# Optimization experiments

Hardware: AMD Instinct MI355X
Metric: run time of the kernel (lower is better)

Reference implementation:

```python
import jax, jax.numpy as jnp
import numpy as np

KERNEL_MUL = 2.0
KERNEL_NUM = 5


def _mmd(source, target):
    n_s = source.shape[0]
    total = jnp.concatenate([source, target], axis=0)  # (2N, D)
    n = total.shape[0]
    # pairwise squared L2 via a^2 + b^2 - 2ab (avoids (2N,2N,D) intermediate)
    sq = jnp.sum(total * total, axis=1)  # (2N,)
    L2 = sq[:, None] + sq[None, :] - 2.0 * (total @ total.T)  # (2N, 2N)
    # torch uses L2_distance.data for bandwidth -> stop_gradient
    bandwidth = jax.lax.stop_gradient(jnp.sum(L2)) / (n * n - n)
    bandwidth = bandwidth / (KERNEL_MUL ** (KERNEL_NUM // 2))
    # multi-bandwidth RBF sum
    kernels = jnp.zeros_like(L2)
    for i in range(KERNEL_NUM):
        kernels = kernels + jnp.exp(-L2 / (bandwidth * KERNEL_MUL ** i))
    XX = kernels[:n_s, :n_s]
    YY = kernels[n_s:, n_s:]
    XY = kernels[:n_s, n_s:]
    YX = kernels[n_s:, :n_s]
    return jnp.mean(XX) + jnp.mean(YY) - jnp.mean(XY) - jnp.mean(YX)


def setup_inputs() -> dict:
    key = jax.random.key(0)
    k1, k2 = jax.random.split(key)
    source = jax.random.normal(k1, (4096, 256), dtype=jnp.float32)
    target = jax.random.normal(k2, (4096, 256), dtype=jnp.float32) + 0.5
    return {"source": source, "target": target}


def reference(source, target):
    return _mmd(source, target)
```

## Files before the change

kernel.cpp:

```cpp
#include <hip/hip_runtime.h>

typedef short bf16x8 __attribute__((ext_vector_type(8)));
typedef float f32x4 __attribute__((ext_vector_type(4)));

#define KDIM 256
#define BT 128
#define BK 64

__device__ __forceinline__ unsigned short f2bf(float f) {
  unsigned u = __float_as_uint(f);
  unsigned r = (u + 0x7fffu + ((u >> 16) & 1u)) >> 16;
  return (unsigned short)r;
}
__device__ __forceinline__ float bf2f(unsigned short b) {
  return __uint_as_float(((unsigned)b) << 16);
}

__device__ __forceinline__ void async_cp16(const void* g, void* l) {
  __builtin_amdgcn_global_load_lds(
      (const __attribute__((address_space(1))) unsigned int*)g,
      (__attribute__((address_space(3))) unsigned int*)l, 16, 0, 0);
}

__global__ __launch_bounds__(256) void mmd_stage(
    const float* __restrict__ src, const float* __restrict__ tgt, int ns,
    unsigned short* __restrict__ Tbf, float* __restrict__ sq,
    float* __restrict__ scol, float* __restrict__ sum_sq) {
  __shared__ float sp[256];
  __shared__ float rw[4];
  int t = threadIdx.x;
  int lane = t & 63, wave = t >> 6;
  sp[t] = 0.f;
  __syncthreads();
  int sub = t & 31;
  int rsel = t >> 5;
  float colacc[8];
#pragma unroll
  for (int j = 0; j < 8; ++j) colacc[j] = 0.f;
  float tsq = 0.f;
#pragma unroll
  for (int it = 0; it < 4; ++it) {
    int r = blockIdx.x * 32 + it * 8 + rsel;
    const float* rp = (r < ns) ? (src + (size_t)r * KDIM)
                               : (tgt + (size_t)(r - ns) * KDIM);
    float4 v0 = *(const float4*)(rp + sub * 8);
    float4 v1 = *(const float4*)(rp + sub * 8 + 4);
    float vals[8] = {v0.x, v0.y, v0.z, v0.w, v1.x, v1.y, v1.z, v1.w};
    unsigned pk[4];
    float ssp = 0.f;
#pragma unroll
    for (int j = 0; j < 4; ++j) {
      unsigned short b0 = f2bf(vals[2 * j]);
      unsigned short b1 = f2bf(vals[2 * j + 1]);
      float x0 = bf2f(b0), x1 = bf2f(b1);
      pk[j] = (unsigned)b0 | ((unsigned)b1 << 16);
      ssp += x0 * x0 + x1 * x1;
      colacc[2 * j] += x0;
      colacc[2 * j + 1] += x1;
    }
    *(uint4*)(Tbf + (size_t)r * KDIM + sub * 8) =
        make_uint4(pk[0], pk[1], pk[2], pk[3]);
    tsq += ssp;
    float ss = ssp;
#pragma unroll
    for (int off = 16; off; off >>= 1) ss += __shfl_down(ss, off, 32);
    if (sub == 0) sq[r] = ss;
  }
#pragma unroll
  for (int j = 0; j < 8; ++j) atomicAdd(&sp[sub * 8 + j], colacc[j]);
#pragma unroll
  for (int off = 32; off; off >>= 1) tsq += __shfl_down(tsq, off, 64);
  if (lane == 0) rw[wave] = tsq;
  __syncthreads();
  atomicAdd(&scol[t], sp[t]);
  if (t == 0) atomicAdd(sum_sq, rw[0] + rw[1] + rw[2] + rw[3]);
}

__global__ void mmd_prep2(const float* __restrict__ scol,
                          const float* __restrict__ sum_sq,
                          float* __restrict__ coef, float* __restrict__ out,
                          int n) {
  int t = threadIdx.x;
  float4 v = *(const float4*)(scol + t * 4);
  float p = v.x * v.x + v.y * v.y + v.z * v.z + v.w * v.w;
#pragma unroll
  for (int off = 32; off; off >>= 1) p += __shfl_down(p, off, 64);
  if (t == 0) {
    double ssq = (double)p;
    double S = (double)sum_sq[0];
    double nn = (double)n;
    double sumL2 = 2.0 * nn * S - 2.0 * ssq;
    double bw = sumL2 / (nn * nn - nn) / 4.0;
    double l2e = 1.4426950408889634;
#pragma unroll
    for (int i = 0; i < 5; ++i)
      coef[i] = (float)(-l2e / (bw * (double)(1 << i)));
    out[0] = 0.f;
  }
}

__device__ __forceinline__ float2 pk_add(float2 a, float2 b) {
  return make_float2(a.x + b.x, a.y + b.y);
}
__device__ __forceinline__ float2 pk_mul(float2 a, float2 b) {
  return make_float2(a.x * b.x, a.y * b.y);
}
__device__ __forceinline__ float2 pk_fma(float2 a, float2 b, float2 c) {
  return make_float2(__builtin_fmaf(a.x, b.x, c.x),
                     __builtin_fmaf(a.y, b.y, c.y));
}

__global__ __launch_bounds__(256) void mmd_main(
    const unsigned short* __restrict__ Tbf, const float* __restrict__ sq,
    const float* __restrict__ coef, float* __restrict__ out, int halfTiles,
    float inv) {
  __shared__ short As[BT * BK];
  __shared__ short Bs[BT * BK];
  __shared__ float sqa[BT];
  __shared__ float sqb[BT];
  __shared__ float red[4];

  int id = blockIdx.x;
  int bi = (int)((sqrtf(8.f * (float)id + 1.f) - 1.f) * 0.5f);
  while ((bi + 1) * (bi + 2) / 2 <= id) ++bi;
  while (bi * (bi + 1) / 2 > id) --bi;
  int bj = id - bi * (bi + 1) / 2;
  int rowBase = bi * BT, colBase = bj * BT;

  int t = threadIdx.x;
  int lane = t & 63, wave = t >> 6;

  if (t < 128) sqa[t] = sq[rowBase + t];
  else sqb[t - 128] = sq[colBase + (t - 128)];

  f32x4 acc[4][4];
#pragma unroll
  for (int a = 0; a < 4; ++a)
#pragma unroll
    for (int b = 0; b < 4; ++b) {
      f32x4 z = {0.f, 0.f, 0.f, 0.f};
      acc[a][b] = z;
    }

  int wrow = (wave >> 1) * 64, wcol = (wave & 1) * 64;
  int lrow = lane >> 3;
  int kgsw = (lane & 7) ^ lrow;
  int frow = lane & 15;
  int kq = lane >> 4;

  for (int c = 0; c < 4; ++c) {
    int k0 = c * BK;
#pragma unroll
    for (int j = 0; j < 4; ++j) {
      int R0 = j * 32 + wave * 8;
      int ldsoff = (j * 256 + wave * 64) * 8;
      async_cp16(Tbf + (size_t)(rowBase + R0 + lrow) * KDIM + k0 + kgsw * 8,
                 &As[ldsoff]);
      async_cp16(Tbf + (size_t)(colBase + R0 + lrow) * KDIM + k0 + kgsw * 8,
                 &Bs[ldsoff]);
    }
    __syncthreads();
#pragma unroll
    for (int ks = 0; ks < 2; ++ks) {
      bf16x8 af[4], bfv[4];
#pragma unroll
      for (int mt = 0; mt < 4; ++mt) {
        int r = wrow + mt * 16 + frow;
        int pg = (ks * 4 + kq) ^ (r & 7);
        af[mt] = *(const bf16x8*)&As[r * BK + pg * 8];
      }
#pragma unroll
      for (int nt = 0; nt < 4; ++nt) {
        int r = wcol + nt * 16 + frow;
        int pg = (ks * 4 + kq) ^ (r & 7);
        bfv[nt] = *(const bf16x8*)&Bs[r * BK + pg * 8];
      }
#pragma unroll
      for (int mt = 0; mt < 4; ++mt)
#pragma unroll
        for (int nt = 0; nt < 4; ++nt)
          acc[mt][nt] = __builtin_amdgcn_mfma_f32_16x16x32_bf16(
              af[mt], bfv[nt], acc[mt][nt], 0, 0, 0);
    }
    __syncthreads();
  }

  float c4 = coef[4];
  float m2c4 = -2.f * c4;
  float2 m2v = make_float2(m2c4, m2c4);
  int ccol = lane & 15;
  int rb = (lane >> 4) * 4;
  float ra[16];
#pragma unroll
  for (int mt = 0; mt < 4; ++mt)
#pragma unroll
    for (int rg = 0; rg < 4; ++rg)
      ra[mt * 4 + rg] = sqa[wrow + mt * 16 + rb + rg] * c4;
  float cbv[4];
#pragma unroll
  for (int nt = 0; nt < 4; ++nt) cbv[nt] = sqb[wcol + nt * 16 + ccol] * c4;

  float2 lsum2 = make_float2(0.f, 0.f);
#pragma unroll
  for (int mt = 0; mt < 4; ++mt) {
#pragma unroll
    for (int nt = 0; nt < 4; ++nt) {
      float cb = cbv[nt];
#pragma unroll
      for (int rp = 0; rp < 4; rp += 2) {
        float2 g = make_float2(acc[mt][nt][rp], acc[mt][nt][rp + 1]);
        float2 sab = make_float2(ra[mt * 4 + rp] + cb, ra[mt * 4 + rp + 1] + cb);
        float2 u = pk_fma(g, m2v, sab);
        float2 e = make_float2(__builtin_amdgcn_exp2f(u.x),
                               __builtin_amdgcn_exp2f(u.y));
        float2 e2 = pk_mul(e, e);
        float2 e4 = pk_mul(e2, e2);
        float2 e8 = pk_mul(e4, e4);
        float2 s = pk_add(e, e2);
        s = pk_add(s, e4);
        s = pk_add(s, e8);
        s = pk_fma(e8, e8, s);
        lsum2 = pk_add(lsum2, s);
      }
    }
  }
  float lsum = lsum2.x + lsum2.y;
#pragma unroll
  for (int off = 32; off; off >>= 1) lsum += __shfl_down(lsum, off, 64);
  if (lane == 0) red[wave] = lsum;
  __syncthreads();
  if (t == 0) {
    float w = ((bi < halfTiles) == (bj < halfTiles)) ? 1.f : -1.f;
    float f = (bi == bj) ? 1.f : 2.f;
    atomicAdd(out, w * f * inv * (red[0] + red[1] + red[2] + red[3]));
  }
}

extern "C" void kernel_launch(void* const* d_in, const int* in_sizes, int n_in,
                              void* d_out, int out_size, void* d_ws,
                              size_t ws_size, hipStream_t stream) {
  const float* src = (const float*)d_in[0];
  const float* tgt = (const float*)d_in[1];
  int ns = in_sizes[0] / KDIM;
  int ntr = in_sizes[1] / KDIM;
  int n = ns + ntr;

  char* ws = (char*)d_ws;
  unsigned short* Tbf = (unsigned short*)ws;
  size_t off = (size_t)n * KDIM * sizeof(unsigned short);
  float* sq = (float*)(ws + off);     off += (size_t)n * 4;
  float* scol = (float*)(ws + off);   off += (size_t)KDIM * 4;
  float* sum_sq = (float*)(ws + off); off += 4;
  float* coef = (float*)(ws + off);

  hipMemsetAsync(scol, 0, (KDIM + 1) * sizeof(float), stream);

  mmd_stage<<<n / 32, 256, 0, stream>>>(src, tgt, ns, Tbf, sq, scol, sum_sq);
  mmd_prep2<<<1, 64, 0, stream>>>(scol, sum_sq, coef, (float*)d_out, n);
  int nb = n / BT;
  int nblk = nb * (nb + 1) / 2;
  mmd_main<<<nblk, 256, 0, stream>>>(Tbf, sq, coef, (float*)d_out, ns / BT,
                                     1.f / ((float)ns * (float)ns));
}
```

Measured before the change: 110.9 us.

## Fuse stage, bandwidth reduction and main tile loop into one cooperative persistent kernel

```diff
diff --git a/kernel.cpp b/kernel.cpp
--- a/kernel.cpp
+++ b/kernel.cpp
@@ -1,4 +1,7 @@
 #include <hip/hip_runtime.h>
+#include <hip/hip_cooperative_groups.h>
+
+namespace cg = cooperative_groups;
 
 typedef short bf16x8 __attribute__((ext_vector_type(8)));
 typedef float f32x4 __attribute__((ext_vector_type(4)));
@@ -20,6 +23,242 @@
   __builtin_amdgcn_global_load_lds(
       (const __attribute__((address_space(1))) unsigned int*)g,
       (__attribute__((address_space(3))) unsigned int*)l, 16, 0, 0);
+}
+
+__device__ __forceinline__ float2 pk_add(float2 a, float2 b) {
+  return make_float2(a.x + b.x, a.y + b.y);
+}
+__device__ __forceinline__ float2 pk_mul(float2 a, float2 b) {
+  return make_float2(a.x * b.x, a.y * b.y);
+}
+__device__ __forceinline__ float2 pk_fma(float2 a, float2 b, float2 c) {
+  return make_float2(__builtin_fmaf(a.x, b.x, c.x),
+                     __builtin_fmaf(a.y, b.y, c.y));
+}
+
+__global__ __launch_bounds__(256) void mmd_fused(
+    const float* __restrict__ src, const float* __restrict__ tgt, int ns,
+    unsigned short* __restrict__ Tbf, float* __restrict__ sq,
+    float* __restrict__ pscol, float* __restrict__ psums,
+    float* __restrict__ p2col, float* __restrict__ p2s,
+    float* __restrict__ out, int halfTiles, float inv, int nTiles,
+    int nChunks, int n) {
+  __shared__ short As[BT * BK];
+  __shared__ short Bs[BT * BK];
+  __shared__ float sqa[BT];
+  __shared__ float sqb[BT];
+  __shared__ float redS[4];
+  __shared__ float coefS;
+
+  cg::grid_group grid = cg::this_grid();
+  int t = threadIdx.x;
+  int lane = t & 63, wave = t >> 6;
+  int nB = gridDim.x;
+  int blk = blockIdx.x;
+
+  float* sp = (float*)As;
+  sp[t] = 0.f;
+  __syncthreads();
+  int sub = t & 31;
+  int rsel = t >> 5;
+  float colacc[8];
+#pragma unroll
+  for (int j = 0; j < 8; ++j) colacc[j] = 0.f;
+  float tsq = 0.f;
+  for (int cs = blk; cs < nChunks; cs += nB) {
+    int r = cs * 8 + rsel;
+    const float* rp = (r < ns) ? (src + (size_t)r * KDIM)
+                               : (tgt + (size_t)(r - ns) * KDIM);
+    float4 v0 = *(const float4*)(rp + sub * 8);
+    float4 v1 = *(const float4*)(rp + sub * 8 + 4);
+    float vals[8] = {v0.x, v0.y, v0.z, v0.w, v1.x, v1.y, v1.z, v1.w};
+    unsigned pk[4];
+    float ssp = 0.f;
+#pragma unroll
+    for (int j = 0; j < 4; ++j) {
+      unsigned short b0 = f2bf(vals[2 * j]);
+      unsigned short b1 = f2bf(vals[2 * j + 1]);
+      float x0 = bf2f(b0), x1 = bf2f(b1);
+      pk[j] = (unsigned)b0 | ((unsigned)b1 << 16);
+      ssp += x0 * x0 + x1 * x1;
+      colacc[2 * j] += x0;
+      colacc[2 * j + 1] += x1;
+    }
+    *(uint4*)(Tbf + (size_t)r * KDIM + sub * 8) =
+        make_uint4(pk[0], pk[1], pk[2], pk[3]);
+    tsq += ssp;
+    float ss = ssp;
+#pragma unroll
+    for (int off = 16; off; off >>= 1) ss += __shfl_down(ss, off, 32);
+    if (sub == 0) sq[r] = ss;
+  }
+#pragma unroll
+  for (int j = 0; j < 8; ++j) atomicAdd(&sp[sub * 8 + j], colacc[j]);
+#pragma unroll
+  for (int off = 32; off; off >>= 1) tsq += __shfl_down(tsq, off, 64);
+  if (lane == 0) redS[wave] = tsq;
+  __syncthreads();
+  pscol[(size_t)blk * 256 + t] = sp[t];
+  if (t == 0) psums[blk] = redS[0] + redS[1] + redS[2] + redS[3];
+  if (blk == 0 && t == 0) out[0] = 0.f;
+  grid.sync();
+
+  int nred = (nB < 64) ? nB : 64;
+  if (blk < nred) {
+    float a = 0.f;
+    for (int r = blk; r < nB; r += 64) a += pscol[(size_t)r * 256 + t];
+    p2col[blk * 256 + t] = a;
+    if (wave == 0) {
+      float v = 0.f;
+      int r = blk + lane * 64;
+      if (lane < 16 && r < nB) v = psums[r];
+#pragma unroll
+      for (int off = 8; off; off >>= 1) v += __shfl_down(v, off, 64);
+      if (lane == 0) p2s[blk] = v;
+    }
+  }
+  grid.sync();
+
+  {
+    float s = 0.f;
+#pragma unroll 8
+    for (int r = 0; r < nred; ++r) s += p2col[r * 256 + t];
+    float p = s * s;
+#pragma unroll
+    for (int off = 32; off; off >>= 1) p += __shfl_down(p, off, 64);
+    if (lane == 0) redS[wave] = p;
+    float S = 0.f;
+    if (wave == 0) {
+      float v = (lane < nred) ? p2s[lane] : 0.f;
+#pragma unroll
+      for (int off = 32; off; off >>= 1) v += __shfl_down(v, off, 64);
+      S = v;
+    }
+    __syncthreads();
+    if (t == 0) {
+      double ssq = (double)(redS[0] + redS[1] + redS[2] + redS[3]);
+      double Sd = (double)S;
+      double nn = (double)n;
+      double sumL2 = 2.0 * nn * Sd - 2.0 * ssq;
+      double bw = sumL2 / (nn * nn - nn) / 4.0;
+      coefS = (float)(-1.4426950408889634 / (16.0 * bw));
+    }
+    __syncthreads();
+  }
+
+  int wrow = (wave >> 1) * 64, wcol = (wave & 1) * 64;
+  int lrow = lane >> 3;
+  int kgsw = (lane & 7) ^ lrow;
+  int frow = lane & 15;
+  int kq = lane >> 4;
+  int ccol = lane & 15;
+  int rb = (lane >> 4) * 4;
+
+  for (int id = blk; id < nTiles; id += nB) {
+    int bi = (int)((sqrtf(8.f * (float)id + 1.f) - 1.f) * 0.5f);
+    while ((bi + 1) * (bi + 2) / 2 <= id) ++bi;
+    while (bi * (bi + 1) / 2 > id) --bi;
+    int bj = id - bi * (bi + 1) / 2;
+    int rowBase = bi * BT, colBase = bj * BT;
+
+    if (t < 128) sqa[t] = sq[rowBase + t];
+    else sqb[t - 128] = sq[colBase + (t - 128)];
+
+    f32x4 acc[4][4];
+#pragma unroll
+    for (int a = 0; a < 4; ++a)
+#pragma unroll
+      for (int b = 0; b < 4; ++b) {
+        f32x4 z = {0.f, 0.f, 0.f, 0.f};
+        acc[a][b] = z;
+      }
+
+    for (int c = 0; c < 4; ++c) {
+      int k0 = c * BK;
+#pragma unroll
+      for (int j = 0; j < 4; ++j) {
+        int R0 = j * 32 + wave * 8;
+        int ldsoff = (j * 256 + wave * 64) * 8;
+        async_cp16(Tbf + (size_t)(rowBase + R0 + lrow) * KDIM + k0 + kgsw * 8,
+                   &As[ldsoff]);
+        async_cp16(Tbf + (size_t)(colBase + R0 + lrow) * KDIM + k0 + kgsw * 8,
+                   &Bs[ldsoff]);
+      }
+      __syncthreads();
+#pragma unroll
+      for (int ks = 0; ks < 2; ++ks) {
+        bf16x8 af[4], bfv[4];
+#pragma unroll
+        for (int mt = 0; mt < 4; ++mt) {
+          int r = wrow + mt * 16 + frow;
+          int pg = (ks * 4 + kq) ^ (r & 7);
+          af[mt] = *(const bf16x8*)&As[r * BK + pg * 8];
+        }
+#pragma unroll
+        for (int nt = 0; nt < 4; ++nt) {
+          int r = wcol + nt * 16 + frow;
+          int pg = (ks * 4 + kq) ^ (r & 7);
+          bfv[nt] = *(const bf16x8*)&Bs[r * BK + pg * 8];
+        }
+#pragma unroll
+        for (int mt = 0; mt < 4; ++mt)
+#pragma unroll
+          for (int nt = 0; nt < 4; ++nt)
+            acc[mt][nt] = __builtin_amdgcn_mfma_f32_16x16x32_bf16(
+                af[mt], bfv[nt], acc[mt][nt], 0, 0, 0);
+      }
+      __syncthreads();
+    }
+
+    float c4 = coefS;
+    float m2c4 = -2.f * c4;
+    float2 m2v = make_float2(m2c4, m2c4);
+    float ra[16];
+#pragma unroll
+    for (int mt = 0; mt < 4; ++mt)
+#pragma unroll
+      for (int rg = 0; rg < 4; ++rg)
+        ra[mt * 4 + rg] = sqa[wrow + mt * 16 + rb + rg] * c4;
+    float cbv[4];
+#pragma unroll
+    for (int nt = 0; nt < 4; ++nt) cbv[nt] = sqb[wcol + nt * 16 + ccol] * c4;
+
+    float2 lsum2 = make_float2(0.f, 0.f);
+#pragma unroll
+    for (int mt = 0; mt < 4; ++mt) {
+#pragma unroll
+      for (int nt = 0; nt < 4; ++nt) {
+        float cb = cbv[nt];
+#pragma unroll
+        for (int rp = 0; rp < 4; rp += 2) {
+          float2 g = make_float2(acc[mt][nt][rp], acc[mt][nt][rp + 1]);
+          float2 sab =
+              make_float2(ra[mt * 4 + rp] + cb, ra[mt * 4 + rp + 1] + cb);
+          float2 u = pk_fma(g, m2v, sab);
+          float2 e = make_float2(__builtin_amdgcn_exp2f(u.x),
+                                 __builtin_amdgcn_exp2f(u.y));
+          float2 e2 = pk_mul(e, e);
+          float2 e4 = pk_mul(e2, e2);
+          float2 e8 = pk_mul(e4, e4);
+          float2 s = pk_add(e, e2);
+          s = pk_add(s, e4);
+          s = pk_add(s, e8);
+          s = pk_fma(e8, e8, s);
+          lsum2 = pk_add(lsum2, s);
+        }
+      }
+    }
+    float lsum = lsum2.x + lsum2.y;
+#pragma unroll
+    for (int off = 32; off; off >>= 1) lsum += __shfl_down(lsum, off, 64);
+    if (lane == 0) redS[wave] = lsum;
+    __syncthreads();
+    if (t == 0) {
+      float w = ((bi < halfTiles) == (bj < halfTiles)) ? 1.f : -1.f;
+      float f = (bi == bj) ? 1.f : 2.f;
+      atomicAdd(out, w * f * inv * (redS[0] + redS[1] + redS[2] + redS[3]));
+    }
+  }
 }
 
 __global__ __launch_bounds__(256) void mmd_stage(
@@ -32,8 +271,7 @@
   int lane = t & 63, wave = t >> 6;
   sp[t] = 0.f;
   __syncthreads();
-  int sub = t & 31;
-  int rsel = t >> 5;
+  int sub = t & 31, rsel = t >> 5;
   float colacc[8];
 #pragma unroll
   for (int j = 0; j < 8; ++j) colacc[j] = 0.f;
@@ -91,23 +329,9 @@
     double nn = (double)n;
     double sumL2 = 2.0 * nn * S - 2.0 * ssq;
     double bw = sumL2 / (nn * nn - nn) / 4.0;
-    double l2e = 1.4426950408889634;
-#pragma unroll
-    for (int i = 0; i < 5; ++i)
-      coef[i] = (float)(-l2e / (bw * (double)(1 << i)));
+    coef[0] = (float)(-1.4426950408889634 / (16.0 * bw));
     out[0] = 0.f;
   }
-}
-
-__device__ __forceinline__ float2 pk_add(float2 a, float2 b) {
-  return make_float2(a.x + b.x, a.y + b.y);
-}
-__device__ __forceinline__ float2 pk_mul(float2 a, float2 b) {
-  return make_float2(a.x * b.x, a.y * b.y);
-}
-__device__ __forceinline__ float2 pk_fma(float2 a, float2 b, float2 c) {
-  return make_float2(__builtin_fmaf(a.x, b.x, c.x),
-                     __builtin_fmaf(a.y, b.y, c.y));
 }
 
 __global__ __launch_bounds__(256) void mmd_main(
@@ -185,7 +409,7 @@
     __syncthreads();
   }
 
-  float c4 = coef[4];
+  float c4 = coef[0];
   float m2c4 = -2.f * c4;
   float2 m2v = make_float2(m2c4, m2c4);
   int ccol = lane & 15;
@@ -209,7 +433,8 @@
 #pragma unroll
       for (int rp = 0; rp < 4; rp += 2) {
         float2 g = make_float2(acc[mt][nt][rp], acc[mt][nt][rp + 1]);
-        float2 sab = make_float2(ra[mt * 4 + rp] + cb, ra[mt * 4 + rp + 1] + cb);
+        float2 sab =
+            make_float2(ra[mt * 4 + rp] + cb, ra[mt * 4 + rp + 1] + cb);
         float2 u = pk_fma(g, m2v, sab);
         float2 e = make_float2(__builtin_amdgcn_exp2f(u.x),
                                __builtin_amdgcn_exp2f(u.y));
@@ -248,17 +473,40 @@
   char* ws = (char*)d_ws;
   unsigned short* Tbf = (unsigned short*)ws;
   size_t off = (size_t)n * KDIM * sizeof(unsigned short);
-  float* sq = (float*)(ws + off);     off += (size_t)n * 4;
-  float* scol = (float*)(ws + off);   off += (size_t)KDIM * 4;
-  float* sum_sq = (float*)(ws + off); off += 4;
-  float* coef = (float*)(ws + off);
-
-  hipMemsetAsync(scol, 0, (KDIM + 1) * sizeof(float), stream);
-
-  mmd_stage<<<n / 32, 256, 0, stream>>>(src, tgt, ns, Tbf, sq, scol, sum_sq);
-  mmd_prep2<<<1, 64, 0, stream>>>(scol, sum_sq, coef, (float*)d_out, n);
+  float* sq = (float*)(ws + off);    off += (size_t)n * 4;
+  float* pscol = (float*)(ws + off); off += (size_t)1024 * 256 * 4;
+  float* psums = (float*)(ws + off); off += 1024 * 4;
+  float* p2col = (float*)(ws + off); off += 64 * 256 * 4;
+  float* p2s = (float*)(ws + off);   off += 64 * 4;
+  float* scolF = (float*)(ws + off); off += 256 * 4;
+  float* sumsqF = (float*)(ws + off); off += 4;
+  float* coefF = (float*)(ws + off);
+
+  float* out = (float*)d_out;
   int nb = n / BT;
-  int nblk = nb * (nb + 1) / 2;
-  mmd_main<<<nblk, 256, 0, stream>>>(Tbf, sq, coef, (float*)d_out, ns / BT,
-                                     1.f / ((float)ns * (float)ns));
-}
+  int nTiles = nb * (nb + 1) / 2;
+  int nChunks = n / 8;
+  int halfTiles = ns / BT;
+  float inv = 1.f / ((float)ns * (float)ns);
+
+  int mb = 0;
+  hipOccupancyMaxActiveBlocksPerMultiprocessor(
+      &mb, reinterpret_cast<const void*>(mmd_fused), 256, 0);
+  if (mb < 1) mb = 1;
+  int grid = 256 * mb;
+  if (grid > 1024) grid = 1024;
+
+  void* args[] = {&src,  &tgt,   &ns,  &Tbf,       &sq,     &pscol, &psums,
+                  &p2col, &p2s,  &out, &halfTiles, &inv,    &nTiles,
+                  &nChunks, &n};
+  hipError_t e = hipLaunchCooperativeKernel(
+      reinterpret_cast<const void*>(mmd_fused), dim3(grid), dim3(256), args, 0,
+      stream);
+  if (e != hipSuccess) {
+    hipMemsetAsync(scolF, 0, 257 * sizeof(float), stream);
+    mmd_stage<<<n / 32, 256, 0, stream>>>(src, tgt, ns, Tbf, sq, scolF,
+                                          sumsqF);
+    mmd_prep2<<<1, 64, 0, stream>>>(scolF, sumsqF, coefF, out, n);
+    mmd_main<<<nTiles, 256, 0, stream>>>(Tbf, sq, coefF, out, halfTiles, inv);
+  }
+}
```

Result: slower. 182.3 us (+64.4%).
